# Optimization experiments

Measured on AMD Instinct MI355X. Metric: run time of the kernel, lower is better.

## Reference

```python
import jax, jax.numpy as jnp
import numpy as np

H, KV, D, EPS = 16, 8, 128, 1e-6

def _rms(t, w):
    # per-head RMSNorm over last dim, computed in fp32
    t32 = t.astype(jnp.float32)
    return (w * t32 * jax.lax.rsqrt(jnp.mean(t32 * t32, axis=-1, keepdims=True) + EPS)).astype(t.dtype)

def _rotate_half(t):
    h = t.shape[-1] // 2
    return jnp.concatenate([-t[..., h:], t[..., :h]], axis=-1)

def setup_inputs() -> dict:
    key = jax.random.key(0)
    ks = jax.random.split(key, 8)
    B, S, HS = 4, 2048, 2048
    return {
        'x': jax.random.normal(ks[0], (B, S, HS), dtype=jnp.float32),
        'cos': jax.random.uniform(ks[1], (S, D), dtype=jnp.float32),
        'sin': jax.random.uniform(ks[2], (S, D), dtype=jnp.float32),
        'wq': jax.random.normal(ks[3], (H * D, HS), dtype=jnp.float32) * 0.02,
        'wk': jax.random.normal(ks[4], (KV * D, HS), dtype=jnp.float32) * 0.02,
        'wv': jax.random.normal(ks[5], (KV * D, HS), dtype=jnp.float32) * 0.02,
        'wo': jax.random.normal(ks[6], (HS, H * D), dtype=jnp.float32) * 0.02,
        'q_norm_w': jnp.ones((D,), dtype=jnp.float32),
        'k_norm_w': jnp.ones((D,), dtype=jnp.float32),
    }

def reference(x, cos, sin, wq, wk, wv, wo, q_norm_w, k_norm_w):
    B, S, _ = x.shape
    n_rep = H // KV
    # QKV projections (torch Linear: x @ W^T)
    xq = (x @ wq.T).reshape(B, S, H, D)
    xk = (x @ wk.T).reshape(B, S, KV, D)
    xv = (x @ wv.T).reshape(B, S, KV, D)
    # per-head RMSNorm on q/k
    xq = _rms(xq, q_norm_w)
    xk = _rms(xk, k_norm_w)
    # RoPE: cos/sin [S, D] broadcast over batch and heads
    c = cos[None, :, None, :]
    s = sin[None, :, None, :]
    xq = xq * c + _rotate_half(xq) * s
    xk = xk * c + _rotate_half(xk) * s
    # GQA: repeat kv heads, move heads forward -> [B, H, S, D]
    xq = xq.transpose(0, 2, 1, 3)
    xk = jnp.repeat(xk, n_rep, axis=2).transpose(0, 2, 1, 3)
    xv = jnp.repeat(xv, n_rep, axis=2).transpose(0, 2, 1, 3)
    # causal softmax attention
    scores = jnp.einsum('bhqd,bhkd->bhqk', xq, xk) / jnp.sqrt(jnp.float32(D))
    causal = jnp.tril(jnp.ones((S, S), dtype=bool))
    scores = jnp.where(causal, scores, -jnp.inf)
    attn = jax.nn.softmax(scores, axis=-1)
    out = jnp.einsum('bhqk,bhkd->bhqd', attn, xv)
    out = out.transpose(0, 2, 1, 3).reshape(B, S, H * D)
    return out @ wo.T
```

## Files before the change

kernel.cpp:

```cpp
#include <hip/hip_runtime.h>
#include <hip/hip_bf16.h>
#include <stdint.h>

using bf16 = __hip_bfloat16;
typedef __attribute__((ext_vector_type(8))) short bf16x8;
typedef __attribute__((ext_vector_type(4))) float f32x4;
typedef __attribute__((ext_vector_type(8))) unsigned short ushort8;

#define MFMA16(a,b,c) __builtin_amdgcn_mfma_f32_16x16x32_bf16(a,b,c,0,0,0)

static constexpr int Bc = 4, Sc = 2048, HSc = 2048, Hc = 16, KVc = 8, Dc = 128;

__device__ __forceinline__ void gl_lds16(const void* g, void* l) {
  __builtin_amdgcn_global_load_lds((const __attribute__((address_space(1))) uint32_t*)g,
                                   (__attribute__((address_space(3))) uint32_t*)l, 16, 0, 0);
}

__device__ __forceinline__ unsigned short f2bf(float f) {
  bf16 h = __float2bfloat16(f);
  return *reinterpret_cast<unsigned short*>(&h);
}

__global__ __launch_bounds__(256) void cvt_all(const float* __restrict__ x,
                                               const float* __restrict__ wq,
                                               const float* __restrict__ wk,
                                               const float* __restrict__ wv,
                                               const float* __restrict__ wo,
                                               unsigned short* __restrict__ xb,
                                               unsigned short* __restrict__ wqkv,
                                               unsigned short* __restrict__ wob) {
  const int NX = 2097152, NQ = 524288, NK = 262144, NV = 262144, NO = 524288;
  const int T = NX + NQ + NK + NV + NO;
  int stride = gridDim.x * blockDim.x;
  for (int i = blockIdx.x * blockDim.x + threadIdx.x; i < T; i += stride) {
    const float* s;
    unsigned short* d;
    int j = i;
    if (j < NX) { s = x; d = xb; }
    else if ((j -= NX) < NQ) { s = wq; d = wqkv; }
    else if ((j -= NQ) < NK) { s = wk; d = wqkv + (size_t)NQ * 8; }
    else if ((j -= NK) < NV) { s = wv; d = wqkv + (size_t)(NQ + NK) * 8; }
    else { j -= NV; s = wo; d = wob; }
    const float4 a = *(const float4*)(s + (size_t)j * 8);
    const float4 b = *(const float4*)(s + (size_t)j * 8 + 4);
    ushort8 o;
    o[0] = f2bf(a.x); o[1] = f2bf(a.y); o[2] = f2bf(a.z); o[3] = f2bf(a.w);
    o[4] = f2bf(b.x); o[5] = f2bf(b.y); o[6] = f2bf(b.z); o[7] = f2bf(b.w);
    *(ushort8*)(d + (size_t)j * 8) = o;
  }
}

__device__ __forceinline__ void storeC(float* C, size_t i, float v) { C[i] = v; }
__device__ __forceinline__ void storeC(bf16* C, size_t i, float v) { C[i] = __float2bfloat16(v); }

#define LDA_(MI, BUF)                                                          \
  _Pragma("unroll") for (int rf = 0; rf < 4; ++rf)                             \
  _Pragma("unroll") for (int k = 0; k < 2; ++k) {                              \
    const int row_ = (MI * 4 + rf) * 16 + lr;                                  \
    a[rf][k] = *(const bf16x8*)&sA[BUF][wm][row_][((k * 4 + lg) ^ (row_ & 7)) * 8]; \
  }
#define LDB_(NI, BUF, BREG)                                                    \
  _Pragma("unroll") for (int j = 0; j < 2; ++j)                                \
  _Pragma("unroll") for (int k = 0; k < 2; ++k) {                              \
    const int row_ = (bco + NI * 2 + j) * 16 + lr;                             \
    BREG[j][k] = *(const bf16x8*)&sB[BUF][bh][row_][((k * 4 + lg) ^ (row_ & 7)) * 8]; \
  }
#define MM_(MI, NI, BREG)                                                      \
  __builtin_amdgcn_s_setprio(1);                                               \
  _Pragma("unroll") for (int rf = 0; rf < 4; ++rf)                             \
  _Pragma("unroll") for (int j = 0; j < 2; ++j)                                \
  _Pragma("unroll") for (int k = 0; k < 2; ++k)                                \
    acc[MI * 4 + rf][NI * 2 + j] =                                             \
        MFMA16(a[rf][k], BREG[j][k], acc[MI * 4 + rf][NI * 2 + j]);            \
  __builtin_amdgcn_s_setprio(0);
#define BAR_ __builtin_amdgcn_s_barrier();
#define VM4_ asm volatile("s_waitcnt vmcnt(4)" ::: "memory");
#define VM0_ asm volatile("s_waitcnt vmcnt(0)" ::: "memory");

template <typename OUT_T>
__global__ __launch_bounds__(512, 2) void gemm8(const bf16* __restrict__ A,
                                                const bf16* __restrict__ B,
                                                OUT_T* __restrict__ C,
                                                int M, int N, int K,
                                                int gm, int gn, int rbm, int rbn) {
  const int nwg = gridDim.x;
  const int cpx = nwg >> 3;
  const int swz = (blockIdx.x & 7) * cpx + (blockIdx.x >> 3);
  const int rsz = rbm * rbn;
  const int region = swz / rsz, rid = swz % rsz;
  const int regions_n = gn / rbn;
  const int bm = (region / regions_n) * rbm + rid / rbn;
  const int bn = (region % regions_n) * rbn + rid % rbn;

  __shared__ __align__(16) bf16 sA[2][2][128][64];
  __shared__ __align__(16) bf16 sB[2][2][128][64];

  const int tid = threadIdx.x;
  const int lane = tid & 63;
  const int wave = tid >> 6;
  const int wm = wave >> 2;
  const int wn = wave & 3;
  const int lg = lane >> 4, lr = lane & 15;
  const int bh = wn >> 1;
  const int bco = (wn & 1) * 4;

  const int rowA = bm * 256;
  const int colB = bn * 256;
  const int NT = K >> 6;

  f32x4 acc[8][4];
  #pragma unroll
  for (int i = 0; i < 8; ++i)
    #pragma unroll
    for (int j = 0; j < 4; ++j) acc[i][j] = (f32x4){0.f, 0.f, 0.f, 0.f};

  auto stA = [&](int buf, int half, int kt) {
    const bf16* src = A + (size_t)(rowA + half * 128) * K + kt * 64;
    #pragma unroll
    for (int is = 0; is < 2; ++is) {
      int r = is * 64 + (tid >> 3);
      int sl = (tid & 7) ^ (r & 7);
      gl_lds16(src + (size_t)r * K + sl * 8, &sA[buf][half][r][(tid & 7) * 8]);
    }
  };
  auto stB = [&](int buf, int half, int kt) {
    const bf16* src = B + (size_t)(colB + half * 128) * K + kt * 64;
    #pragma unroll
    for (int is = 0; is < 2; ++is) {
      int r = is * 64 + (tid >> 3);
      int sl = (tid & 7) ^ (r & 7);
      gl_lds16(src + (size_t)r * K + sl * 8, &sB[buf][half][r][(tid & 7) * 8]);
    }
  };

  stB(0, 0, 0); stB(0, 1, 0); stA(0, 0, 0); stA(0, 1, 0);
  stB(1, 0, 1); stB(1, 1, 1);
  VM4_
  __builtin_amdgcn_s_barrier();

  for (int t = 0; t < NT; t += 2) {
    const bool lastit = (t + 2 >= NT);
    bf16x8 a[4][2], bl[2][2], br[2][2];
    LDA_(0, 0) LDB_(0, 0, bl)
    stA(1, 0, t + 1);
    BAR_ MM_(0, 0, bl) BAR_
    LDB_(1, 0, br)
    stA(1, 1, t + 1);
    BAR_ MM_(0, 1, br) BAR_
    LDA_(1, 0)
    if (!lastit) stB(0, 0, t + 2);
    BAR_ MM_(1, 0, bl) BAR_
    if (!lastit) stB(0, 1, t + 2);
    BAR_ MM_(1, 1, br)
    if (lastit) { VM0_ } else { VM4_ }
    BAR_
    LDA_(0, 1) LDB_(0, 1, bl)
    if (!lastit) stA(0, 0, t + 2);
    BAR_ MM_(0, 0, bl) BAR_
    LDB_(1, 1, br)
    if (!lastit) stA(0, 1, t + 2);
    BAR_ MM_(0, 1, br) BAR_
    LDA_(1, 1)
    if (t + 3 < NT) stB(1, 0, t + 3);
    BAR_ MM_(1, 0, bl) BAR_
    if (t + 3 < NT) stB(1, 1, t + 3);
    BAR_ MM_(1, 1, br)
    if (!lastit) { VM4_ }
    BAR_
  }

  #pragma unroll
  for (int rf = 0; rf < 8; ++rf)
    #pragma unroll
    for (int cf = 0; cf < 4; ++cf)
      #pragma unroll
      for (int r = 0; r < 4; ++r) {
        size_t row = rowA + wm * 128 + rf * 16 + lg * 4 + r;
        size_t col = colB + wn * 64 + cf * 16 + lr;
        storeC(C, row * (size_t)N + col, acc[rf][cf][r]);
      }
}

__global__ __launch_bounds__(256) void norm_rope(const bf16* __restrict__ qkv,
                                                 const float* __restrict__ cosT,
                                                 const float* __restrict__ sinT,
                                                 const float* __restrict__ qw,
                                                 const float* __restrict__ kw,
                                                 bf16* __restrict__ Qn, bf16* __restrict__ Kn) {
  const int bs = blockIdx.x;
  const int s = bs & (Sc - 1);
  const int b = bs >> 11;
  const int wave = threadIdx.x >> 6, lane = threadIdx.x & 63;
  const float QSCL = 0.08838834764831845f * 1.4426950408889634f;
  const float c0 = cosT[(size_t)s * Dc + lane];
  const float c1 = cosT[(size_t)s * Dc + 64 + lane];
  const float s0 = sinT[(size_t)s * Dc + lane];
  const float s1 = sinT[(size_t)s * Dc + 64 + lane];
  const bf16* row = qkv + (size_t)bs * 4096;
  #pragma unroll
  for (int i = 0; i < 6; ++i) {
    int head = wave * 6 + i;
    bool isQ = head < 16;
    int col = head * Dc;
    float x0 = __bfloat162float(row[col + lane]);
    float x1 = __bfloat162float(row[col + 64 + lane]);
    float ss = x0 * x0 + x1 * x1;
    #pragma unroll
    for (int off = 32; off; off >>= 1) ss += __shfl_xor(ss, off);
    float inv = rsqrtf(ss * (1.0f / 128.0f) + 1e-6f);
    const float* w = isQ ? qw : kw;
    float n0 = x0 * inv * w[lane];
    float n1 = x1 * inv * w[lane + 64];
    float o0 = n0 * c0 - n1 * s0;
    float o1 = n1 * c1 + n0 * s1;
    if (isQ) { o0 *= QSCL; o1 *= QSCL; }
    size_t base;
    bf16* dst;
    if (isQ) { base = ((size_t)(b * Hc + head) * Sc + s) * Dc; dst = Qn; }
    else     { base = ((size_t)(b * KVc + (head - 16)) * Sc + s) * Dc; dst = Kn; }
    dst[base + lane] = __float2bfloat16(o0);
    dst[base + 64 + lane] = __float2bfloat16(o1);
  }
}

__global__ __launch_bounds__(256) void v_transpose(const bf16* __restrict__ qkv,
                                                   bf16* __restrict__ Vt) {
  const int s0 = blockIdx.x * 64;
  const int bk = blockIdx.y;
  __shared__ __align__(16) bf16 tile[64][136];
  const int tid = threadIdx.x;
  const size_t srcbase = ((size_t)(bk >> 3) * Sc + s0) * 4096 + 3072 + (size_t)(bk & 7) * Dc;
  #pragma unroll
  for (int it = 0; it < 4; ++it) {
    int idx = it * 256 + tid;
    int r = idx >> 4, ch = idx & 15;
    *(bf16x8*)&tile[r][ch * 8] = *(const bf16x8*)(qkv + srcbase + (size_t)r * 4096 + ch * 8);
  }
  __syncthreads();
  const size_t dstbase = (size_t)bk * Dc * Sc + s0;
  #pragma unroll
  for (int it = 0; it < 4; ++it) {
    int idx = it * 256 + tid;
    int d = idx >> 3, scc = idx & 7;
    bf16x8 o;
    #pragma unroll
    for (int j = 0; j < 8; ++j) o[j] = *(const short*)&tile[scc * 8 + j][d];
    *(bf16x8*)(Vt + dstbase + (size_t)d * Sc + scc * 8) = o;
  }
}

__global__ __launch_bounds__(512, 4) void flash_kernel(const bf16* __restrict__ Qn,
                                                       const bf16* __restrict__ Kn,
                                                       const bf16* __restrict__ Vt,
                                                       bf16* __restrict__ Out) {
  const int qi = 15 - (blockIdx.x >> 6);
  const int bh = blockIdx.x & 63;
  const int q0 = qi * 128;
  const int b = bh >> 4, h = bh & 15;
  const int kv = h >> 1;
  const int tid = threadIdx.x;
  const int wave = tid >> 6, lane = tid & 63;
  const int lg = lane >> 4, lr = lane & 15;
  const int rm = lr & 7;

  __shared__ __align__(16) bf16 sK[64][128];
  __shared__ __align__(16) bf16 sV[128][64];
  __shared__ __align__(16) bf16 sP[8][16][72];

  const int qrow = q0 + wave * 16;
  const bf16* qbase = Qn + ((size_t)(b * Hc + h) * Sc + qrow + lr) * Dc;
  bf16x8 qf[4];
  #pragma unroll
  for (int kk = 0; kk < 4; ++kk) qf[kk] = *(const bf16x8*)(qbase + kk * 32 + lg * 8);

  f32x4 oacc[8];
  #pragma unroll
  for (int i = 0; i < 8; ++i) oacc[i] = (f32x4){0.f, 0.f, 0.f, 0.f};
  float m_run[4], l_run[4];
  #pragma unroll
  for (int r = 0; r < 4; ++r) { m_run[r] = -3.0e38f; l_run[r] = 0.f; }

  const bf16* kb = Kn + ((size_t)(b * KVc + kv) * Sc) * Dc;
  const bf16* vb = Vt + ((size_t)(b * KVc + kv) * Dc) * Sc;

  const int nt = 2 * qi + 2;
  for (int t = 0; t < nt; ++t) {
    const int k0 = t * 64;
    #pragma unroll
    for (int it = 0; it < 2; ++it) {
      int idx = it * 512 + tid;
      int r = idx >> 4, ps = idx & 15;
      int ls = ps ^ (r & 7);
      gl_lds16(kb + (size_t)(k0 + r) * Dc + ls * 8, &sK[r][ps * 8]);
    }
    #pragma unroll
    for (int it = 0; it < 2; ++it) {
      int idx = it * 512 + tid;
      int r = idx >> 3, ps = idx & 7;
      int ls = ps ^ (r & 7);
      gl_lds16(vb + (size_t)r * Sc + k0 + ls * 8, &sV[r][ps * 8]);
    }
    __syncthreads();

    float tt[4][4];
    __builtin_amdgcn_s_setprio(1);
    #pragma unroll
    for (int c = 0; c < 4; ++c) {
      f32x4 sacc = (f32x4){0.f, 0.f, 0.f, 0.f};
      #pragma unroll
      for (int kk = 0; kk < 4; ++kk) {
        bf16x8 kf = *(const bf16x8*)&sK[c * 16 + lr][((kk * 4 + lg) ^ rm) * 8];
        sacc = MFMA16(qf[kk], kf, sacc);
      }
      if (k0 + c * 16 + 15 <= qrow) {
        #pragma unroll
        for (int r = 0; r < 4; ++r) tt[c][r] = sacc[r];
      } else {
        int kg = k0 + c * 16 + lr;
        #pragma unroll
        for (int r = 0; r < 4; ++r) {
          int qg = qrow + lg * 4 + r;
          tt[c][r] = (kg <= qg) ? sacc[r] : -3.0e38f;
        }
      }
    }
    __builtin_amdgcn_s_setprio(0);

    float pmax[4];
    #pragma unroll
    for (int r = 0; r < 4; ++r) {
      float mx = fmaxf(fmaxf(tt[0][r], tt[1][r]), fmaxf(tt[2][r], tt[3][r]));
      mx = fmaxf(mx, __shfl_xor(mx, 1));
      mx = fmaxf(mx, __shfl_xor(mx, 2));
      mx = fmaxf(mx, __shfl_xor(mx, 4));
      mx = fmaxf(mx, __shfl_xor(mx, 8));
      pmax[r] = mx;
    }
    bool grow = (pmax[0] > m_run[0] + 8.f) || (pmax[1] > m_run[1] + 8.f) ||
                (pmax[2] > m_run[2] + 8.f) || (pmax[3] > m_run[3] + 8.f);
    if (__any(grow)) {
      #pragma unroll
      for (int r = 0; r < 4; ++r) {
        float mnew = fmaxf(m_run[r], pmax[r]);
        float alpha = exp2f(m_run[r] - mnew);
        m_run[r] = mnew;
        l_run[r] *= alpha;
        #pragma unroll
        for (int dc = 0; dc < 8; ++dc) oacc[dc][r] *= alpha;
      }
    }
    #pragma unroll
    for (int r = 0; r < 4; ++r) {
      float local = 0.f;
      #pragma unroll
      for (int c = 0; c < 4; ++c) { tt[c][r] = exp2f(tt[c][r] - m_run[r]); local += tt[c][r]; }
      l_run[r] += local;
    }
    #pragma unroll
    for (int c = 0; c < 4; ++c)
      #pragma unroll
      for (int r = 0; r < 4; ++r)
        sP[wave][lg * 4 + r][c * 16 + lr] = __float2bfloat16(tt[c][r]);

    __builtin_amdgcn_s_setprio(1);
    #pragma unroll
    for (int kk2 = 0; kk2 < 2; ++kk2) {
      bf16x8 pf = *(const bf16x8*)&sP[wave][lr][kk2 * 32 + lg * 8];
      #pragma unroll
      for (int dc = 0; dc < 8; ++dc) {
        bf16x8 vf = *(const bf16x8*)&sV[dc * 16 + lr][((kk2 * 4 + lg) ^ rm) * 8];
        oacc[dc] = MFMA16(pf, vf, oacc[dc]);
      }
    }
    __builtin_amdgcn_s_setprio(0);

    __syncthreads();
  }

  #pragma unroll
  for (int r = 0; r < 4; ++r) {
    float l = l_run[r];
    l += __shfl_xor(l, 1);
    l += __shfl_xor(l, 2);
    l += __shfl_xor(l, 4);
    l += __shfl_xor(l, 8);
    l_run[r] = 1.f / l;
  }
  #pragma unroll
  for (int dc = 0; dc < 8; ++dc)
    #pragma unroll
    for (int r = 0; r < 4; ++r) {
      size_t row = (size_t)b * Sc + qrow + lg * 4 + r;
      Out[row * (size_t)(Hc * Dc) + h * Dc + dc * 16 + lr] =
          __float2bfloat16(oacc[dc][r] * l_run[r]);
    }
}

extern "C" void kernel_launch(void* const* d_in, const int* in_sizes, int n_in,
                              void* d_out, int out_size, void* d_ws, size_t ws_size,
                              hipStream_t stream) {
  const float* x    = (const float*)d_in[0];
  const float* cosT = (const float*)d_in[1];
  const float* sinT = (const float*)d_in[2];
  const float* wq   = (const float*)d_in[3];
  const float* wk   = (const float*)d_in[4];
  const float* wv   = (const float*)d_in[5];
  const float* wo   = (const float*)d_in[6];
  const float* qnw  = (const float*)d_in[7];
  const float* knw  = (const float*)d_in[8];
  float* out = (float*)d_out;

  const size_t MB = 1ull << 20;
  char* ws = (char*)d_ws;
  bf16* xb   = (bf16*)(ws + 0);
  bf16* wqkv = (bf16*)(ws + 32 * MB);
  bf16* wob  = (bf16*)(ws + 48 * MB);
  bf16* qkv  = (bf16*)(ws + 56 * MB);
  bf16* Qn   = (bf16*)(ws + 120 * MB);
  bf16* Kn   = (bf16*)(ws + 152 * MB);
  bf16* Vt   = (bf16*)(ws + 168 * MB);
  bf16* attn = (bf16*)(ws + 184 * MB);

  cvt_all<<<2048, 256, 0, stream>>>(x, wq, wk, wv, wo,
                                    (unsigned short*)xb, (unsigned short*)wqkv,
                                    (unsigned short*)wob);

  gemm8<bf16><<<512, 512, 0, stream>>>(xb, wqkv, qkv, 8192, 4096, 2048, 32, 16, 16, 4);
  norm_rope<<<8192, 256, 0, stream>>>(qkv, cosT, sinT, qnw, knw, Qn, Kn);
  v_transpose<<<dim3(32, 32), 256, 0, stream>>>(qkv, Vt);
  flash_kernel<<<1024, 512, 0, stream>>>(Qn, Kn, Vt, attn);
  gemm8<float><<<256, 512, 0, stream>>>(attn, wob, out, 8192, 2048, 2048, 32, 8, 8, 4);
}
```

Before: 385.9 us.

## Transpose QK^T MFMA so each lane owns one query row for softmax

Swaps the MFMA operands so the score tile comes out transposed, with each lane holding one query row across four key columns. The per-row max and sum then need two cross-lane shuffles instead of four reductions of four shuffles each, and the softmax state shrinks to one scalar per lane. P is written to LDS with packed 2-element stores into a XOR-swizzled layout, which is meant to avoid bank conflicts. The cost is extra shuffles to broadcast the rescale factors back to the output accumulator layout, and more complex P indexing.

```diff
diff --git a/kernel.cpp b/kernel.cpp
--- a/kernel.cpp
+++ b/kernel.cpp
@@ -265,7 +265,7 @@
 
   __shared__ __align__(16) bf16 sK[64][128];
   __shared__ __align__(16) bf16 sV[128][64];
-  __shared__ __align__(16) bf16 sP[8][16][72];
+  __shared__ __align__(16) unsigned short sP[8][16][72];
 
   const int qrow = q0 + wave * 16;
   const bf16* qbase = Qn + ((size_t)(b * Hc + h) * Sc + qrow + lr) * Dc;
@@ -276,9 +276,7 @@
   f32x4 oacc[8];
   #pragma unroll
   for (int i = 0; i < 8; ++i) oacc[i] = (f32x4){0.f, 0.f, 0.f, 0.f};
-  float m_run[4], l_run[4];
-  #pragma unroll
-  for (int r = 0; r < 4; ++r) { m_run[r] = -3.0e38f; l_run[r] = 0.f; }
+  float m_run = -3.0e38f, l_run = 0.f;
 
   const bf16* kb = Kn + ((size_t)(b * KVc + kv) * Sc) * Dc;
   const bf16* vb = Vt + ((size_t)(b * KVc + kv) * Dc) * Sc;
@@ -303,6 +301,7 @@
     __syncthreads();
 
     float tt[4][4];
+    const int qg = qrow + lr;
     __builtin_amdgcn_s_setprio(1);
     #pragma unroll
     for (int c = 0; c < 4; ++c) {
@@ -310,62 +309,67 @@
       #pragma unroll
       for (int kk = 0; kk < 4; ++kk) {
         bf16x8 kf = *(const bf16x8*)&sK[c * 16 + lr][((kk * 4 + lg) ^ rm) * 8];
-        sacc = MFMA16(qf[kk], kf, sacc);
+        sacc = MFMA16(kf, qf[kk], sacc);
       }
       if (k0 + c * 16 + 15 <= qrow) {
         #pragma unroll
         for (int r = 0; r < 4; ++r) tt[c][r] = sacc[r];
       } else {
-        int kg = k0 + c * 16 + lr;
         #pragma unroll
         for (int r = 0; r < 4; ++r) {
-          int qg = qrow + lg * 4 + r;
+          int kg = k0 + c * 16 + lg * 4 + r;
           tt[c][r] = (kg <= qg) ? sacc[r] : -3.0e38f;
         }
       }
     }
     __builtin_amdgcn_s_setprio(0);
 
-    float pmax[4];
-    #pragma unroll
-    for (int r = 0; r < 4; ++r) {
-      float mx = fmaxf(fmaxf(tt[0][r], tt[1][r]), fmaxf(tt[2][r], tt[3][r]));
-      mx = fmaxf(mx, __shfl_xor(mx, 1));
-      mx = fmaxf(mx, __shfl_xor(mx, 2));
-      mx = fmaxf(mx, __shfl_xor(mx, 4));
-      mx = fmaxf(mx, __shfl_xor(mx, 8));
-      pmax[r] = mx;
-    }
-    bool grow = (pmax[0] > m_run[0] + 8.f) || (pmax[1] > m_run[1] + 8.f) ||
-                (pmax[2] > m_run[2] + 8.f) || (pmax[3] > m_run[3] + 8.f);
+    float m0 = fmaxf(fmaxf(tt[0][0], tt[0][1]), fmaxf(tt[0][2], tt[0][3]));
+    float m1 = fmaxf(fmaxf(tt[1][0], tt[1][1]), fmaxf(tt[1][2], tt[1][3]));
+    float m2 = fmaxf(fmaxf(tt[2][0], tt[2][1]), fmaxf(tt[2][2], tt[2][3]));
+    float m3 = fmaxf(fmaxf(tt[3][0], tt[3][1]), fmaxf(tt[3][2], tt[3][3]));
+    float mx = fmaxf(fmaxf(m0, m1), fmaxf(m2, m3));
+    mx = fmaxf(mx, __shfl_xor(mx, 16));
+    mx = fmaxf(mx, __shfl_xor(mx, 32));
+
+    bool grow = mx > m_run + 8.f;
     if (__any(grow)) {
-      #pragma unroll
-      for (int r = 0; r < 4; ++r) {
-        float mnew = fmaxf(m_run[r], pmax[r]);
-        float alpha = exp2f(m_run[r] - mnew);
-        m_run[r] = mnew;
-        l_run[r] *= alpha;
-        #pragma unroll
-        for (int dc = 0; dc < 8; ++dc) oacc[dc][r] *= alpha;
-      }
-    }
-    #pragma unroll
-    for (int r = 0; r < 4; ++r) {
-      float local = 0.f;
-      #pragma unroll
-      for (int c = 0; c < 4; ++c) { tt[c][r] = exp2f(tt[c][r] - m_run[r]); local += tt[c][r]; }
-      l_run[r] += local;
-    }
+      float mnew = fmaxf(m_run, mx);
+      float alpha = exp2f(m_run - mnew);
+      m_run = mnew;
+      l_run *= alpha;
+      float a0 = __shfl(alpha, lg * 4 + 0);
+      float a1 = __shfl(alpha, lg * 4 + 1);
+      float a2 = __shfl(alpha, lg * 4 + 2);
+      float a3 = __shfl(alpha, lg * 4 + 3);
+      #pragma unroll
+      for (int dc = 0; dc < 8; ++dc) {
+        oacc[dc][0] *= a0; oacc[dc][1] *= a1; oacc[dc][2] *= a2; oacc[dc][3] *= a3;
+      }
+    }
+    float lsum = 0.f;
     #pragma unroll
     for (int c = 0; c < 4; ++c)
       #pragma unroll
-      for (int r = 0; r < 4; ++r)
-        sP[wave][lg * 4 + r][c * 16 + lr] = __float2bfloat16(tt[c][r]);
+      for (int r = 0; r < 4; ++r) { tt[c][r] = exp2f(tt[c][r] - m_run); lsum += tt[c][r]; }
+    l_run += lsum;
+
+    #pragma unroll
+    for (int c = 0; c < 4; ++c)
+      #pragma unroll
+      for (int r2 = 0; r2 < 2; ++r2) {
+        int col = c * 16 + lg * 4 + 2 * r2;
+        int colx = (((col >> 3) ^ rm) << 3) + (col & 7);
+        ushort2 w;
+        w.x = f2bf(tt[c][2 * r2]);
+        w.y = f2bf(tt[c][2 * r2 + 1]);
+        *(ushort2*)&sP[wave][lr][colx] = w;
+      }
 
     __builtin_amdgcn_s_setprio(1);
     #pragma unroll
     for (int kk2 = 0; kk2 < 2; ++kk2) {
-      bf16x8 pf = *(const bf16x8*)&sP[wave][lr][kk2 * 32 + lg * 8];
+      bf16x8 pf = *(const bf16x8*)&sP[wave][lr][((kk2 * 4 + lg) ^ rm) * 8];
       #pragma unroll
       for (int dc = 0; dc < 8; ++dc) {
         bf16x8 vf = *(const bf16x8*)&sV[dc * 16 + lr][((kk2 * 4 + lg) ^ rm) * 8];
@@ -377,23 +381,23 @@
     __syncthreads();
   }
 
-  #pragma unroll
-  for (int r = 0; r < 4; ++r) {
-    float l = l_run[r];
-    l += __shfl_xor(l, 1);
-    l += __shfl_xor(l, 2);
-    l += __shfl_xor(l, 4);
-    l += __shfl_xor(l, 8);
-    l_run[r] = 1.f / l;
-  }
-  #pragma unroll
-  for (int dc = 0; dc < 8; ++dc)
-    #pragma unroll
-    for (int r = 0; r < 4; ++r) {
-      size_t row = (size_t)b * Sc + qrow + lg * 4 + r;
-      Out[row * (size_t)(Hc * Dc) + h * Dc + dc * 16 + lr] =
-          __float2bfloat16(oacc[dc][r] * l_run[r]);
-    }
+  float l = l_run;
+  l += __shfl_xor(l, 16);
+  l += __shfl_xor(l, 32);
+  float linv = 1.f / l;
+  float li0 = __shfl(linv, lg * 4 + 0);
+  float li1 = __shfl(linv, lg * 4 + 1);
+  float li2 = __shfl(linv, lg * 4 + 2);
+  float li3 = __shfl(linv, lg * 4 + 3);
+  #pragma unroll
+  for (int dc = 0; dc < 8; ++dc) {
+    size_t rowb = (size_t)b * Sc + qrow + lg * 4;
+    size_t colb = (size_t)h * Dc + dc * 16 + lr;
+    Out[(rowb + 0) * (size_t)(Hc * Dc) + colb] = __float2bfloat16(oacc[dc][0] * li0);
+    Out[(rowb + 1) * (size_t)(Hc * Dc) + colb] = __float2bfloat16(oacc[dc][1] * li1);
+    Out[(rowb + 2) * (size_t)(Hc * Dc) + colb] = __float2bfloat16(oacc[dc][2] * li2);
+    Out[(rowb + 3) * (size_t)(Hc * Dc) + colb] = __float2bfloat16(oacc[dc][3] * li3);
+  }
 }
 
 extern "C" void kernel_launch(void* const* d_in, const int* in_sizes, int n_in,
```

Result: no change. 384.7 us (-0.3%).
